# Optimization experiments

Measured on AMD Instinct MI355X. Metric: run time of the kernel, lower is better.

Reference implementation:

```python
import jax, jax.numpy as jnp
import numpy as np

TOKENS = 2048
HIDDEN = 2048
INTER = 1408
EXPERTS = 16
TOP_K = 2


def setup_inputs() -> dict:
    key = jax.random.key(0)
    k_x, k_g, k_gp, k_up, k_dp = jax.random.split(key, 5)
    s = 0.02  # weight init scale
    return {
        "hidden_states": jax.random.normal(k_x, (TOKENS, HIDDEN), jnp.float32),
        "w_gate": jax.random.normal(k_g, (HIDDEN, EXPERTS), jnp.float32) * s,
        "w_gate_proj": jax.random.normal(k_gp, (EXPERTS, HIDDEN, INTER), jnp.float32) * s,
        "w_up_proj": jax.random.normal(k_up, (EXPERTS, HIDDEN, INTER), jnp.float32) * s,
        "w_down_proj": jax.random.normal(k_dp, (EXPERTS, INTER, HIDDEN), jnp.float32) * s,
    }


def reference(hidden_states, w_gate, w_gate_proj, w_up_proj, w_down_proj):
    T, H = hidden_states.shape
    E = w_gate.shape[1]
    # --- router: gate linear + top-k sigmoid routing (fused_topk_sigmoid) ---
    router_logits = hidden_states @ w_gate                      # [T, E]
    scores = jax.nn.sigmoid(router_logits.astype(jnp.float32))  # [T, E]
    topk_w, topk_ids = jax.lax.top_k(scores, TOP_K)             # [T, K]
    topk_w = topk_w / topk_w.sum(axis=-1, keepdims=True)        # renormalize (norm_topk_prob)
    # dense combine weights [T, E]: zero for unselected experts
    cw = jnp.zeros((T, E), jnp.float32).at[jnp.arange(T)[:, None], topk_ids].set(topk_w)
    # --- experts: SwiGLU MLP per expert, combined by routing weights ---
    g = jnp.einsum('th,ehi->eti', hidden_states, w_gate_proj)   # [E, T, I]
    u = jnp.einsum('th,ehi->eti', hidden_states, w_up_proj)     # [E, T, I]
    h = jax.nn.silu(g) * u                                      # [E, T, I]
    y = jnp.einsum('eti,eih->eth', h, w_down_proj)              # [E, T, H]
    out = jnp.einsum('eth,te->th', y, cw.astype(hidden_states.dtype))
    return out
```

## Files before the change

kernel.cpp:

```cpp
#include <hip/hip_runtime.h>
#include <stdint.h>

#define TOKENS 2048
#define HIDDEN 2048
#define INTER  1408
#define NEXP   16
#define BK     64

using bf16x8 = __attribute__((ext_vector_type(8))) __bf16;
using f32x8  = __attribute__((ext_vector_type(8))) float;
using f32x4  = __attribute__((ext_vector_type(4))) float;

__device__ __forceinline__ unsigned short bf16bits(float f) {
    union { __bf16 h; unsigned short u; } cv;
    cv.h = (__bf16)f;
    return cv.u;
}

__device__ __forceinline__ void cvt_store8(const f32x8& s, unsigned short* dst) {
    bf16x8 v;
#pragma unroll
    for (int j = 0; j < 8; j++) v[j] = (__bf16)s[j];
    *(bf16x8*)dst = v;
}

__global__ __launch_bounds__(64) void router_kernel(
    const float* __restrict__ x, const float* __restrict__ wg,
    int* __restrict__ cnt, int* __restrict__ tok, float* __restrict__ wts,
    unsigned short* __restrict__ xbf)
{
    const int t = blockIdx.x;
    const int lane = threadIdx.x;
    float acc[NEXP];
#pragma unroll
    for (int e = 0; e < NEXP; e++) acc[e] = 0.f;
    const float* xr = x + (size_t)t * HIDDEN;
    unsigned short* xbr = xbf + (size_t)t * HIDDEN;
    for (int h = lane; h < HIDDEN; h += 64) {
        const float xv = xr[h];
        xbr[h] = bf16bits(xv);
        const float* wr = wg + (size_t)h * NEXP;
#pragma unroll
        for (int e = 0; e < NEXP; e++) acc[e] += xv * wr[e];
    }
#pragma unroll
    for (int off = 32; off > 0; off >>= 1) {
#pragma unroll
        for (int e = 0; e < NEXP; e++) acc[e] += __shfl_down(acc[e], off, 64);
    }
    if (lane == 0) {
        float s[NEXP];
#pragma unroll
        for (int e = 0; e < NEXP; e++) s[e] = 1.f / (1.f + __expf(-acc[e]));
        int i0 = 0;
#pragma unroll
        for (int e = 1; e < NEXP; e++) if (s[e] > s[i0]) i0 = e;
        int i1 = (i0 == 0) ? 1 : 0;
#pragma unroll
        for (int e = 0; e < NEXP; e++) if (e != i0 && s[e] > s[i1]) i1 = e;
        float w0 = s[i0], w1 = s[i1];
        const float inv = 1.f / (w0 + w1);
        w0 *= inv; w1 *= inv;
        const int s0 = atomicAdd(&cnt[i0], 1);
        tok[i0 * TOKENS + s0] = t * 2;
        wts[i0 * TOKENS + s0] = w0;
        const int s1 = atomicAdd(&cnt[i1], 1);
        tok[i1 * TOKENS + s1] = t * 2 + 1;
        wts[i1 * TOKENS + s1] = w1;
    }
}

#define LOADVEC8(dstv, baseptr, koff, ldstride)                         \
    do {                                                                \
        const float* _s = (baseptr) + (size_t)(koff) * (ldstride);      \
        _Pragma("unroll")                                               \
        for (int _j = 0; _j < 8; _j++) dstv[_j] = _s[(size_t)_j * (ldstride)]; \
    } while (0)

__global__ __launch_bounds__(256, 2) void gemm1_kernel(
    const unsigned short* __restrict__ xbf, const float* __restrict__ wgp,
    const float* __restrict__ wup, const int* __restrict__ cnt,
    const int* __restrict__ tok, unsigned short* __restrict__ hbuf)
{
    const int e = blockIdx.z;
    const int ne = cnt[e];
    const int m0 = blockIdx.y * 128;
    if (m0 >= ne) return;
    const int n0 = blockIdx.x * 64;

    __shared__ __align__(16) unsigned short As[128 * 64];
    __shared__ __align__(16) unsigned short Bs[2][64 * 64];
    __shared__ int rowp[128];

    const int tid = threadIdx.x;
    if (tid < 128) {
        const int slot = m0 + tid;
        rowp[tid] = tok[e * TOKENS + (slot < ne ? slot : ne - 1)];
    }
    __syncthreads();

    const int lane = tid & 63;
    const int w    = tid >> 6;
    const int wm = (w >> 1) * 64;
    const int wn = (w & 1) * 32;
    const int lr = lane & 15;
    const int lq = lane >> 4;

    const int ac  = tid & 7;
    const int ar0 = tid >> 3;
    const unsigned short* asrc0 = xbf + (size_t)(rowp[ar0     ] >> 1) * HIDDEN + ac * 8;
    const unsigned short* asrc1 = xbf + (size_t)(rowp[ar0 + 32] >> 1) * HIDDEN + ac * 8;
    const unsigned short* asrc2 = xbf + (size_t)(rowp[ar0 + 64] >> 1) * HIDDEN + ac * 8;
    const unsigned short* asrc3 = xbf + (size_t)(rowp[ar0 + 96] >> 1) * HIDDEN + ac * 8;
    const int asw = (ac ^ (ar0 & 7)) * 8;
    unsigned short* adst0 = &As[(ar0     ) * 64 + asw];
    unsigned short* adst1 = &As[(ar0 + 32) * 64 + asw];
    unsigned short* adst2 = &As[(ar0 + 64) * 64 + asw];
    unsigned short* adst3 = &As[(ar0 + 96) * 64 + asw];

    const int bn = lane;
    const int bk = w;
    const float* bsg = wgp + (size_t)e * HIDDEN * INTER + n0 + bn;
    const float* bsu = wup + (size_t)e * HIDDEN * INTER + n0 + bn;
    unsigned short* bdg0 = &Bs[0][bn * 64 + ((bk    ) ^ (bn & 7)) * 8];
    unsigned short* bdg1 = &Bs[0][bn * 64 + ((bk + 4) ^ (bn & 7)) * 8];
    unsigned short* bdu0 = &Bs[1][bn * 64 + ((bk    ) ^ (bn & 7)) * 8];
    unsigned short* bdu1 = &Bs[1][bn * 64 + ((bk + 4) ^ (bn & 7)) * 8];

    f32x4 accg[4][2], accu[4][2];
    const f32x4 z4 = {0.f, 0.f, 0.f, 0.f};
#pragma unroll
    for (int a = 0; a < 4; a++)
#pragma unroll
        for (int b = 0; b < 2; b++) { accg[a][b] = z4; accu[a][b] = z4; }

    f32x8 pg0, pg1, pu0, pu1;
    LOADVEC8(pg0, bsg, bk * 8,        INTER);
    LOADVEC8(pg1, bsg, bk * 8 + 32,   INTER);
    LOADVEC8(pu0, bsu, bk * 8,        INTER);
    LOADVEC8(pu1, bsu, bk * 8 + 32,   INTER);

    for (int k0 = 0; k0 < HIDDEN; k0 += BK) {
        const uint4 a0 = *(const uint4*)(asrc0 + k0);
        const uint4 a1 = *(const uint4*)(asrc1 + k0);
        const uint4 a2 = *(const uint4*)(asrc2 + k0);
        const uint4 a3 = *(const uint4*)(asrc3 + k0);
        *(uint4*)adst0 = a0;
        *(uint4*)adst1 = a1;
        *(uint4*)adst2 = a2;
        *(uint4*)adst3 = a3;
        cvt_store8(pg0, bdg0);
        cvt_store8(pg1, bdg1);
        cvt_store8(pu0, bdu0);
        cvt_store8(pu1, bdu1);
        __syncthreads();

        if (k0 + BK < HIDDEN) {
            LOADVEC8(pg0, bsg, k0 + BK + bk * 8,      INTER);
            LOADVEC8(pg1, bsg, k0 + BK + bk * 8 + 32, INTER);
            LOADVEC8(pu0, bsu, k0 + BK + bk * 8,      INTER);
            LOADVEC8(pu1, bsu, k0 + BK + bk * 8 + 32, INTER);
        }

#pragma unroll
        for (int ks = 0; ks < 2; ks++) {
            bf16x8 af[4], bg[2], bu[2];
#pragma unroll
            for (int tm = 0; tm < 4; tm++) {
                const int r = wm + tm * 16 + lr;
                af[tm] = *(const bf16x8*)&As[r * 64 + (((ks * 4 + lq) ^ (lr & 7)) * 8)];
            }
#pragma unroll
            for (int tn = 0; tn < 2; tn++) {
                const int r = wn + tn * 16 + lr;
                const int off = r * 64 + (((ks * 4 + lq) ^ (lr & 7)) * 8);
                bg[tn] = *(const bf16x8*)&Bs[0][off];
                bu[tn] = *(const bf16x8*)&Bs[1][off];
            }
#pragma unroll
            for (int tm = 0; tm < 4; tm++)
#pragma unroll
                for (int tn = 0; tn < 2; tn++) {
                    accg[tm][tn] = __builtin_amdgcn_mfma_f32_16x16x32_bf16(af[tm], bg[tn], accg[tm][tn], 0, 0, 0);
                    accu[tm][tn] = __builtin_amdgcn_mfma_f32_16x16x32_bf16(af[tm], bu[tn], accu[tm][tn], 0, 0, 0);
                }
        }
        __syncthreads();
    }

#pragma unroll
    for (int tm = 0; tm < 4; tm++)
#pragma unroll
        for (int tn = 0; tn < 2; tn++)
#pragma unroll
            for (int r = 0; r < 4; r++) {
                const int rowL = wm + tm * 16 + lq * 4 + r;
                const int slot = m0 + rowL;
                if (slot < ne) {
                    const int p = rowp[rowL];
                    const int col = n0 + wn + tn * 16 + lr;
                    const float g = accg[tm][tn][r];
                    const float u = accu[tm][tn][r];
                    const float hv = g * u / (1.f + __expf(-g));
                    hbuf[(size_t)p * INTER + col] = bf16bits(hv);
                }
            }
}

__global__ __launch_bounds__(256, 2) void gemm2_kernel(
    const unsigned short* __restrict__ hbuf, const float* __restrict__ wdp,
    const int* __restrict__ cnt, const int* __restrict__ tok,
    const float* __restrict__ wts, float* __restrict__ out)
{
    const int e = blockIdx.z;
    const int ne = cnt[e];
    const int m0 = blockIdx.y * 128;
    if (m0 >= ne) return;
    const int n0 = blockIdx.x * 64;

    __shared__ __align__(16) unsigned short As[128 * 64];
    __shared__ __align__(16) unsigned short Bs[64 * 64];
    __shared__ int rowp[128];
    __shared__ float roww[128];

    const int tid = threadIdx.x;
    if (tid < 128) {
        const int slot = m0 + tid;
        const int cs = slot < ne ? slot : ne - 1;
        rowp[tid] = tok[e * TOKENS + cs];
        roww[tid] = wts[e * TOKENS + cs];
    }
    __syncthreads();

    const int lane = tid & 63;
    const int w    = tid >> 6;
    const int wm = (w >> 1) * 64;
    const int wn = (w & 1) * 32;
    const int lr = lane & 15;
    const int lq = lane >> 4;

    const int ac  = tid & 7;
    const int ar0 = tid >> 3;
    const unsigned short* asrc0 = hbuf + (size_t)rowp[ar0     ] * INTER + ac * 8;
    const unsigned short* asrc1 = hbuf + (size_t)rowp[ar0 + 32] * INTER + ac * 8;
    const unsigned short* asrc2 = hbuf + (size_t)rowp[ar0 + 64] * INTER + ac * 8;
    const unsigned short* asrc3 = hbuf + (size_t)rowp[ar0 + 96] * INTER + ac * 8;
    const int asw = (ac ^ (ar0 & 7)) * 8;
    unsigned short* adst0 = &As[(ar0     ) * 64 + asw];
    unsigned short* adst1 = &As[(ar0 + 32) * 64 + asw];
    unsigned short* adst2 = &As[(ar0 + 64) * 64 + asw];
    unsigned short* adst3 = &As[(ar0 + 96) * 64 + asw];

    const int bn = lane;
    const int bk = w;
    const float* bsd = wdp + (size_t)e * INTER * HIDDEN + n0 + bn;
    unsigned short* bdd0 = &Bs[bn * 64 + ((bk    ) ^ (bn & 7)) * 8];
    unsigned short* bdd1 = &Bs[bn * 64 + ((bk + 4) ^ (bn & 7)) * 8];

    f32x4 acc[4][2];
    const f32x4 z4 = {0.f, 0.f, 0.f, 0.f};
#pragma unroll
    for (int a = 0; a < 4; a++)
#pragma unroll
        for (int b = 0; b < 2; b++) acc[a][b] = z4;

    f32x8 pd0, pd1;
    LOADVEC8(pd0, bsd, bk * 8,      HIDDEN);
    LOADVEC8(pd1, bsd, bk * 8 + 32, HIDDEN);

    for (int k0 = 0; k0 < INTER; k0 += BK) {
        const uint4 a0 = *(const uint4*)(asrc0 + k0);
        const uint4 a1 = *(const uint4*)(asrc1 + k0);
        const uint4 a2 = *(const uint4*)(asrc2 + k0);
        const uint4 a3 = *(const uint4*)(asrc3 + k0);
        *(uint4*)adst0 = a0;
        *(uint4*)adst1 = a1;
        *(uint4*)adst2 = a2;
        *(uint4*)adst3 = a3;
        cvt_store8(pd0, bdd0);
        cvt_store8(pd1, bdd1);
        __syncthreads();

        if (k0 + BK < INTER) {
            LOADVEC8(pd0, bsd, k0 + BK + bk * 8,      HIDDEN);
            LOADVEC8(pd1, bsd, k0 + BK + bk * 8 + 32, HIDDEN);
        }

#pragma unroll
        for (int ks = 0; ks < 2; ks++) {
            bf16x8 af[4], bb[2];
#pragma unroll
            for (int tm = 0; tm < 4; tm++) {
                const int r = wm + tm * 16 + lr;
                af[tm] = *(const bf16x8*)&As[r * 64 + (((ks * 4 + lq) ^ (lr & 7)) * 8)];
            }
#pragma unroll
            for (int tn = 0; tn < 2; tn++) {
                const int r = wn + tn * 16 + lr;
                bb[tn] = *(const bf16x8*)&Bs[r * 64 + (((ks * 4 + lq) ^ (lr & 7)) * 8)];
            }
#pragma unroll
            for (int tm = 0; tm < 4; tm++)
#pragma unroll
                for (int tn = 0; tn < 2; tn++)
                    acc[tm][tn] = __builtin_amdgcn_mfma_f32_16x16x32_bf16(af[tm], bb[tn], acc[tm][tn], 0, 0, 0);
        }
        __syncthreads();
    }

#pragma unroll
    for (int tm = 0; tm < 4; tm++)
#pragma unroll
        for (int tn = 0; tn < 2; tn++)
#pragma unroll
            for (int r = 0; r < 4; r++) {
                const int rowL = wm + tm * 16 + lq * 4 + r;
                const int slot = m0 + rowL;
                if (slot < ne) {
                    const int t = rowp[rowL] >> 1;
                    const float wv = roww[rowL];
                    atomicAdd(&out[(size_t)t * HIDDEN + n0 + wn + tn * 16 + lr],
                              wv * acc[tm][tn][r]);
                }
            }
}

extern "C" void kernel_launch(void* const* d_in, const int* in_sizes, int n_in,
                              void* d_out, int out_size, void* d_ws, size_t ws_size,
                              hipStream_t stream) {
    const float* x   = (const float*)d_in[0];
    const float* wg  = (const float*)d_in[1];
    const float* wgp = (const float*)d_in[2];
    const float* wup = (const float*)d_in[3];
    const float* wdp = (const float*)d_in[4];
    float* out = (float*)d_out;

    char* ws = (char*)d_ws;
    int*   cnt  = (int*)ws;
    int*   tok  = (int*)(ws + 256);
    float* wts  = (float*)(ws + 256 + 131072);
    unsigned short* xbf  = (unsigned short*)(ws + 262400);
    unsigned short* hbuf = (unsigned short*)(ws + 262400 + 8388608);

    hipMemsetAsync(cnt, 0, NEXP * sizeof(int), stream);
    hipMemsetAsync(out, 0, (size_t)TOKENS * HIDDEN * sizeof(float), stream);

    router_kernel<<<dim3(TOKENS), dim3(64), 0, stream>>>(x, wg, cnt, tok, wts, xbf);

    dim3 g1(INTER / 64, TOKENS / 128, NEXP);
    gemm1_kernel<<<g1, dim3(256), 0, stream>>>(xbf, wgp, wup, cnt, tok, hbuf);

    dim3 g2(HIDDEN / 64, TOKENS / 128, NEXP);
    gemm2_kernel<<<g2, dim3(256), 0, stream>>>(hbuf, wdp, cnt, tok, wts, out);
}
```

Baseline: 688.8 us.

## Compact expert tile schedule and deepen register prefetch in both MoE GEMMs

Adds a single-thread schedule kernel that lists only the non-empty (expert, m-tile) pairs, up to 48 entries. Both GEMMs launch over this compact list instead of a 3D grid where most blocks exit immediately. The main loops are unrolled by two with two register sets of fp32 weights in flight, plus an A-tile prefetch issued one stage ahead. MFMA phases raise wave priority with s_setprio, and barriers use explicit lgkmcnt waits. This aims to hide global weight-load latency and cut empty-block launch overhead, at the cost of more registers and an extra tiny kernel launch.

```diff
diff --git a/kernel.cpp b/kernel.cpp
--- a/kernel.cpp
+++ b/kernel.cpp
@@ -6,6 +6,7 @@
 #define INTER  1408
 #define NEXP   16
 #define BK     64
+#define MAXTILES 48
 
 using bf16x8 = __attribute__((ext_vector_type(8))) __bf16;
 using f32x8  = __attribute__((ext_vector_type(8))) float;
@@ -70,6 +71,22 @@
     }
 }
 
+__global__ __launch_bounds__(64) void schedule_kernel(const int* __restrict__ cnt,
+                                                      int* __restrict__ tiles)
+{
+    if (threadIdx.x == 0) {
+        int p = 0;
+        for (int e = 0; e < NEXP; e++) {
+            const int nt = (cnt[e] + 127) >> 7;
+            for (int m = 0; m < nt; m++) {
+                if (p < MAXTILES) tiles[p] = (e << 16) | m;
+                p++;
+            }
+        }
+        for (; p < MAXTILES; p++) tiles[p] = -1;
+    }
+}
+
 #define LOADVEC8(dstv, baseptr, koff, ldstride)                         \
     do {                                                                \
         const float* _s = (baseptr) + (size_t)(koff) * (ldstride);      \
@@ -77,15 +94,42 @@
         for (int _j = 0; _j < 8; _j++) dstv[_j] = _s[(size_t)_j * (ldstride)]; \
     } while (0)
 
+#define G_LOADA(k)                                                      \
+    do {                                                                \
+        a0 = *(const uint4*)(asrc0 + (k));                              \
+        a1 = *(const uint4*)(asrc1 + (k));                              \
+        a2 = *(const uint4*)(asrc2 + (k));                              \
+        a3 = *(const uint4*)(asrc3 + (k));                              \
+    } while (0)
+#define G_STAGEA()                                                      \
+    do {                                                                \
+        *(uint4*)adst0 = a0; *(uint4*)adst1 = a1;                       \
+        *(uint4*)adst2 = a2; *(uint4*)adst3 = a3;                       \
+    } while (0)
+
+#define FENCE_LGKM_BAR()                                                \
+    do {                                                                \
+        asm volatile("s_waitcnt lgkmcnt(0)" ::: "memory");              \
+        __builtin_amdgcn_s_barrier();                                   \
+    } while (0)
+#define FENCE_BAR2()                                                    \
+    do {                                                                \
+        asm volatile("" ::: "memory");                                  \
+        __builtin_amdgcn_s_barrier();                                   \
+        asm volatile("" ::: "memory");                                  \
+    } while (0)
+
 __global__ __launch_bounds__(256, 2) void gemm1_kernel(
     const unsigned short* __restrict__ xbf, const float* __restrict__ wgp,
     const float* __restrict__ wup, const int* __restrict__ cnt,
-    const int* __restrict__ tok, unsigned short* __restrict__ hbuf)
+    const int* __restrict__ tok, const int* __restrict__ tiles,
+    unsigned short* __restrict__ hbuf)
 {
-    const int e = blockIdx.z;
+    const int te = tiles[blockIdx.y];
+    if (te < 0) return;
+    const int e  = te >> 16;
+    const int m0 = (te & 0xffff) << 7;
     const int ne = cnt[e];
-    const int m0 = blockIdx.y * 128;
-    if (m0 >= ne) return;
     const int n0 = blockIdx.x * 64;
 
     __shared__ __align__(16) unsigned short As[128 * 64];
@@ -134,58 +178,81 @@
 #pragma unroll
         for (int b = 0; b < 2; b++) { accg[a][b] = z4; accu[a][b] = z4; }
 
-    f32x8 pg0, pg1, pu0, pu1;
-    LOADVEC8(pg0, bsg, bk * 8,        INTER);
-    LOADVEC8(pg1, bsg, bk * 8 + 32,   INTER);
-    LOADVEC8(pu0, bsu, bk * 8,        INTER);
-    LOADVEC8(pu1, bsu, bk * 8 + 32,   INTER);
-
-    for (int k0 = 0; k0 < HIDDEN; k0 += BK) {
-        const uint4 a0 = *(const uint4*)(asrc0 + k0);
-        const uint4 a1 = *(const uint4*)(asrc1 + k0);
-        const uint4 a2 = *(const uint4*)(asrc2 + k0);
-        const uint4 a3 = *(const uint4*)(asrc3 + k0);
-        *(uint4*)adst0 = a0;
-        *(uint4*)adst1 = a1;
-        *(uint4*)adst2 = a2;
-        *(uint4*)adst3 = a3;
-        cvt_store8(pg0, bdg0);
-        cvt_store8(pg1, bdg1);
-        cvt_store8(pu0, bdu0);
-        cvt_store8(pu1, bdu1);
-        __syncthreads();
-
-        if (k0 + BK < HIDDEN) {
-            LOADVEC8(pg0, bsg, k0 + BK + bk * 8,      INTER);
-            LOADVEC8(pg1, bsg, k0 + BK + bk * 8 + 32, INTER);
-            LOADVEC8(pu0, bsu, k0 + BK + bk * 8,      INTER);
-            LOADVEC8(pu1, bsu, k0 + BK + bk * 8 + 32, INTER);
+    uint4 a0, a1, a2, a3;
+    f32x8 pgX0, pgX1, puX0, puX1;
+    f32x8 pgY0, pgY1, puY0, puY1;
+
+    LOADVEC8(pgX0, bsg, bk * 8,        INTER);
+    LOADVEC8(pgX1, bsg, bk * 8 + 32,   INTER);
+    LOADVEC8(puX0, bsu, bk * 8,        INTER);
+    LOADVEC8(puX1, bsu, bk * 8 + 32,   INTER);
+    G_LOADA(0);
+    LOADVEC8(pgY0, bsg, BK + bk * 8,        INTER);
+    LOADVEC8(pgY1, bsg, BK + bk * 8 + 32,   INTER);
+    LOADVEC8(puY0, bsu, BK + bk * 8,        INTER);
+    LOADVEC8(puY1, bsu, BK + bk * 8 + 32,   INTER);
+
+#define G1_MFMA_PHASE()                                                           \
+    do {                                                                          \
+        __builtin_amdgcn_s_setprio(1);                                            \
+        _Pragma("unroll")                                                         \
+        for (int ks = 0; ks < 2; ks++) {                                          \
+            bf16x8 af[4], bg[2], bu[2];                                           \
+            _Pragma("unroll")                                                     \
+            for (int tm = 0; tm < 4; tm++) {                                      \
+                const int r = wm + tm * 16 + lr;                                  \
+                af[tm] = *(const bf16x8*)&As[r * 64 + (((ks * 4 + lq) ^ (lr & 7)) * 8)]; \
+            }                                                                     \
+            _Pragma("unroll")                                                     \
+            for (int tn = 0; tn < 2; tn++) {                                      \
+                const int r = wn + tn * 16 + lr;                                  \
+                const int off = r * 64 + (((ks * 4 + lq) ^ (lr & 7)) * 8);        \
+                bg[tn] = *(const bf16x8*)&Bs[0][off];                             \
+                bu[tn] = *(const bf16x8*)&Bs[1][off];                             \
+            }                                                                     \
+            _Pragma("unroll")                                                     \
+            for (int tm = 0; tm < 4; tm++)                                        \
+                _Pragma("unroll")                                                 \
+                for (int tn = 0; tn < 2; tn++) {                                  \
+                    accg[tm][tn] = __builtin_amdgcn_mfma_f32_16x16x32_bf16(af[tm], bg[tn], accg[tm][tn], 0, 0, 0); \
+                    accu[tm][tn] = __builtin_amdgcn_mfma_f32_16x16x32_bf16(af[tm], bu[tn], accu[tm][tn], 0, 0, 0); \
+                }                                                                 \
+        }                                                                         \
+        __builtin_amdgcn_s_setprio(0);                                            \
+    } while (0)
+
+    for (int k0 = 0; k0 < HIDDEN; k0 += 2 * BK) {
+        G_STAGEA();
+        cvt_store8(pgX0, bdg0);
+        cvt_store8(pgX1, bdg1);
+        cvt_store8(puX0, bdu0);
+        cvt_store8(puX1, bdu1);
+        FENCE_LGKM_BAR();
+        G_LOADA(k0 + BK);
+        if (k0 + 2 * BK < HIDDEN) {
+            LOADVEC8(pgX0, bsg, k0 + 2 * BK + bk * 8,      INTER);
+            LOADVEC8(pgX1, bsg, k0 + 2 * BK + bk * 8 + 32, INTER);
+            LOADVEC8(puX0, bsu, k0 + 2 * BK + bk * 8,      INTER);
+            LOADVEC8(puX1, bsu, k0 + 2 * BK + bk * 8 + 32, INTER);
         }
-
-#pragma unroll
-        for (int ks = 0; ks < 2; ks++) {
-            bf16x8 af[4], bg[2], bu[2];
-#pragma unroll
-            for (int tm = 0; tm < 4; tm++) {
-                const int r = wm + tm * 16 + lr;
-                af[tm] = *(const bf16x8*)&As[r * 64 + (((ks * 4 + lq) ^ (lr & 7)) * 8)];
-            }
-#pragma unroll
-            for (int tn = 0; tn < 2; tn++) {
-                const int r = wn + tn * 16 + lr;
-                const int off = r * 64 + (((ks * 4 + lq) ^ (lr & 7)) * 8);
-                bg[tn] = *(const bf16x8*)&Bs[0][off];
-                bu[tn] = *(const bf16x8*)&Bs[1][off];
-            }
-#pragma unroll
-            for (int tm = 0; tm < 4; tm++)
-#pragma unroll
-                for (int tn = 0; tn < 2; tn++) {
-                    accg[tm][tn] = __builtin_amdgcn_mfma_f32_16x16x32_bf16(af[tm], bg[tn], accg[tm][tn], 0, 0, 0);
-                    accu[tm][tn] = __builtin_amdgcn_mfma_f32_16x16x32_bf16(af[tm], bu[tn], accu[tm][tn], 0, 0, 0);
-                }
+        G1_MFMA_PHASE();
+        FENCE_BAR2();
+
+        G_STAGEA();
+        cvt_store8(pgY0, bdg0);
+        cvt_store8(pgY1, bdg1);
+        cvt_store8(puY0, bdu0);
+        cvt_store8(puY1, bdu1);
+        FENCE_LGKM_BAR();
+        if (k0 + 2 * BK < HIDDEN) G_LOADA(k0 + 2 * BK);
+        if (k0 + 3 * BK < HIDDEN) {
+            LOADVEC8(pgY0, bsg, k0 + 3 * BK + bk * 8,      INTER);
+            LOADVEC8(pgY1, bsg, k0 + 3 * BK + bk * 8 + 32, INTER);
+            LOADVEC8(puY0, bsu, k0 + 3 * BK + bk * 8,      INTER);
+            LOADVEC8(puY1, bsu, k0 + 3 * BK + bk * 8 + 32, INTER);
         }
-        __syncthreads();
+        G1_MFMA_PHASE();
+        FENCE_BAR2();
     }
 
 #pragma unroll
@@ -205,17 +272,20 @@
                     hbuf[(size_t)p * INTER + col] = bf16bits(hv);
                 }
             }
+#undef G1_MFMA_PHASE
 }
 
 __global__ __launch_bounds__(256, 2) void gemm2_kernel(
     const unsigned short* __restrict__ hbuf, const float* __restrict__ wdp,
     const int* __restrict__ cnt, const int* __restrict__ tok,
-    const float* __restrict__ wts, float* __restrict__ out)
+    const float* __restrict__ wts, const int* __restrict__ tiles,
+    float* __restrict__ out)
 {
-    const int e = blockIdx.z;
+    const int te = tiles[blockIdx.y];
+    if (te < 0) return;
+    const int e  = te >> 16;
+    const int m0 = (te & 0xffff) << 7;
     const int ne = cnt[e];
-    const int m0 = blockIdx.y * 128;
-    if (m0 >= ne) return;
     const int n0 = blockIdx.x * 64;
 
     __shared__ __align__(16) unsigned short As[128 * 64];
@@ -264,48 +334,64 @@
 #pragma unroll
         for (int b = 0; b < 2; b++) acc[a][b] = z4;
 
-    f32x8 pd0, pd1;
-    LOADVEC8(pd0, bsd, bk * 8,      HIDDEN);
-    LOADVEC8(pd1, bsd, bk * 8 + 32, HIDDEN);
-
-    for (int k0 = 0; k0 < INTER; k0 += BK) {
-        const uint4 a0 = *(const uint4*)(asrc0 + k0);
-        const uint4 a1 = *(const uint4*)(asrc1 + k0);
-        const uint4 a2 = *(const uint4*)(asrc2 + k0);
-        const uint4 a3 = *(const uint4*)(asrc3 + k0);
-        *(uint4*)adst0 = a0;
-        *(uint4*)adst1 = a1;
-        *(uint4*)adst2 = a2;
-        *(uint4*)adst3 = a3;
-        cvt_store8(pd0, bdd0);
-        cvt_store8(pd1, bdd1);
-        __syncthreads();
-
-        if (k0 + BK < INTER) {
-            LOADVEC8(pd0, bsd, k0 + BK + bk * 8,      HIDDEN);
-            LOADVEC8(pd1, bsd, k0 + BK + bk * 8 + 32, HIDDEN);
+    uint4 a0, a1, a2, a3;
+    f32x8 pdX0, pdX1, pdY0, pdY1;
+
+    LOADVEC8(pdX0, bsd, bk * 8,      HIDDEN);
+    LOADVEC8(pdX1, bsd, bk * 8 + 32, HIDDEN);
+    G_LOADA(0);
+    LOADVEC8(pdY0, bsd, BK + bk * 8,      HIDDEN);
+    LOADVEC8(pdY1, bsd, BK + bk * 8 + 32, HIDDEN);
+
+#define G2_MFMA_PHASE()                                                           \
+    do {                                                                          \
+        __builtin_amdgcn_s_setprio(1);                                            \
+        _Pragma("unroll")                                                         \
+        for (int ks = 0; ks < 2; ks++) {                                          \
+            bf16x8 af[4], bb[2];                                                  \
+            _Pragma("unroll")                                                     \
+            for (int tm = 0; tm < 4; tm++) {                                      \
+                const int r = wm + tm * 16 + lr;                                  \
+                af[tm] = *(const bf16x8*)&As[r * 64 + (((ks * 4 + lq) ^ (lr & 7)) * 8)]; \
+            }                                                                     \
+            _Pragma("unroll")                                                     \
+            for (int tn = 0; tn < 2; tn++) {                                      \
+                const int r = wn + tn * 16 + lr;                                  \
+                bb[tn] = *(const bf16x8*)&Bs[r * 64 + (((ks * 4 + lq) ^ (lr & 7)) * 8)]; \
+            }                                                                     \
+            _Pragma("unroll")                                                     \
+            for (int tm = 0; tm < 4; tm++)                                        \
+                _Pragma("unroll")                                                 \
+                for (int tn = 0; tn < 2; tn++)                                    \
+                    acc[tm][tn] = __builtin_amdgcn_mfma_f32_16x16x32_bf16(af[tm], bb[tn], acc[tm][tn], 0, 0, 0); \
+        }                                                                         \
+        __builtin_amdgcn_s_setprio(0);                                            \
+    } while (0)
+
+    for (int k0 = 0; k0 < INTER; k0 += 2 * BK) {
+        G_STAGEA();
+        cvt_store8(pdX0, bdd0);
+        cvt_store8(pdX1, bdd1);
+        FENCE_LGKM_BAR();
+        G_LOADA(k0 + BK);
+        if (k0 + 2 * BK < INTER) {
+            LOADVEC8(pdX0, bsd, k0 + 2 * BK + bk * 8,      HIDDEN);
+            LOADVEC8(pdX1, bsd, k0 + 2 * BK + bk * 8 + 32, HIDDEN);
         }
-
-#pragma unroll
-        for (int ks = 0; ks < 2; ks++) {
-            bf16x8 af[4], bb[2];
-#pragma unroll
-            for (int tm = 0; tm < 4; tm++) {
-                const int r = wm + tm * 16 + lr;
-                af[tm] = *(const bf16x8*)&As[r * 64 + (((ks * 4 + lq) ^ (lr & 7)) * 8)];
-            }
-#pragma unroll
-            for (int tn = 0; tn < 2; tn++) {
-                const int r = wn + tn * 16 + lr;
-                bb[tn] = *(const bf16x8*)&Bs[r * 64 + (((ks * 4 + lq) ^ (lr & 7)) * 8)];
-            }
-#pragma unroll
-            for (int tm = 0; tm < 4; tm++)
-#pragma unroll
-                for (int tn = 0; tn < 2; tn++)
-                    acc[tm][tn] = __builtin_amdgcn_mfma_f32_16x16x32_bf16(af[tm], bb[tn], acc[tm][tn], 0, 0, 0);
+        G2_MFMA_PHASE();
+        FENCE_BAR2();
+
+        G_STAGEA();
+        cvt_store8(pdY0, bdd0);
+        cvt_store8(pdY1, bdd1);
+        FENCE_LGKM_BAR();
+        if (k0 + 2 * BK < INTER) G_LOADA(k0 + 2 * BK);
+        if (k0 + 3 * BK < INTER) {
+            LOADVEC8(pdY0, bsd, k0 + 3 * BK + bk * 8,      HIDDEN);
+            LOADVEC8(pdY1, bsd, k0 + 3 * BK + bk * 8 + 32, HIDDEN);
         }
-        __syncthreads();
+        G2_MFMA_PHASE();
+        FENCE_BAR2();
     }
 
 #pragma unroll
@@ -323,6 +409,7 @@
                               wv * acc[tm][tn][r]);
                 }
             }
+#undef G2_MFMA_PHASE
 }
 
 extern "C" void kernel_launch(void* const* d_in, const int* in_sizes, int n_in,
@@ -336,7 +423,8 @@
     float* out = (float*)d_out;
 
     char* ws = (char*)d_ws;
-    int*   cnt  = (int*)ws;
+    int*   cnt   = (int*)ws;
+    int*   tiles = (int*)(ws + 64);
     int*   tok  = (int*)(ws + 256);
     float* wts  = (float*)(ws + 256 + 131072);
     unsigned short* xbf  = (unsigned short*)(ws + 262400);
@@ -347,9 +435,11 @@
 
     router_kernel<<<dim3(TOKENS), dim3(64), 0, stream>>>(x, wg, cnt, tok, wts, xbf);
 
-    dim3 g1(INTER / 64, TOKENS / 128, NEXP);
-    gemm1_kernel<<<g1, dim3(256), 0, stream>>>(xbf, wgp, wup, cnt, tok, hbuf);
-
-    dim3 g2(HIDDEN / 64, TOKENS / 128, NEXP);
-    gemm2_kernel<<<g2, dim3(256), 0, stream>>>(hbuf, wdp, cnt, tok, wts, out);
-}
+    schedule_kernel<<<dim3(1), dim3(64), 0, stream>>>(cnt, tiles);
+
+    dim3 g1(INTER / 64, MAXTILES);
+    gemm1_kernel<<<g1, dim3(256), 0, stream>>>(xbf, wgp, wup, cnt, tok, tiles, hbuf);
+
+    dim3 g2(HIDDEN / 64, MAXTILES);
+    gemm2_kernel<<<g2, dim3(256), 0, stream>>>(hbuf, wdp, cnt, tok, wts, tiles, out);
+}
```

Measured after the change: 659.1 us. 4.3% less time.
